# Optimization experiments

Hardware: AMD Instinct MI355X
Metric: run time of the kernel (lower is better)

## Reference

```python
import jax, jax.numpy as jnp
import numpy as np

B, NR, NA, NF = 2, 768, 768, 16
RIN, AIN = 1024, 1024
DIM, HEADS, DHEAD, DEPTH = 512, 8, 64, 4
INNER = HEADS * DHEAD
IFF = int(DIM * 4 * 2 / 3)  # 1365, GEGLU inner dim


def _ln(x, g, b=None):
    mu = jnp.mean(x, axis=-1, keepdims=True)
    var = jnp.mean((x - mu) ** 2, axis=-1, keepdims=True)
    y = (x - mu) * jax.lax.rsqrt(var + 1e-5) * g
    return y if b is None else y + b


def _heads(t):
    b, n, _ = t.shape
    return t.reshape(b, n, HEADS, DHEAD).transpose(0, 2, 1, 3)  # b h n d


def _attend(qx, kvx, wq, wkv, wo, mask):
    q = _heads(qx @ wq) * (DHEAD ** -0.5)
    k, v = map(_heads, jnp.split(kvx @ wkv, 2, axis=-1))
    sim = jnp.einsum('bhid,bhjd->bhij', q, k)
    sim = jnp.where(mask, sim, -jnp.finfo(sim.dtype).max)
    attn = jax.nn.softmax(sim, axis=-1)
    out = jnp.einsum('bhij,bhjd->bhid', attn, v)
    out = out.transpose(0, 2, 1, 3).reshape(qx.shape[0], -1, INNER)
    return out @ wo


def _masks():
    # token types: RNA=0, FUSION=2, ATAC=1, laid out [rna | fusion | atac]
    types = jnp.concatenate([jnp.zeros(NR, jnp.int32), jnp.full((NF,), 2, jnp.int32), jnp.ones(NA, jnp.int32)])
    same = (types[:, None] == types[None, :]).astype(jnp.int32)
    # replicates torch source precedence: (zorro_mask | types_from) == FUSION
    zorro = (same | types[:, None]) == 2
    rt = jnp.arange(3, dtype=jnp.int32)  # return token types (RNA, ATAC, FUSION)
    pm = (rt[:, None] == types[None, :]).astype(jnp.int32)
    # replicates source precedence: (pool_mask | return_types) == GLOBAL(3)
    pool = (pm | rt[:, None]) == 3
    return zorro[None, None], pool[None, None]


def setup_inputs() -> dict:
    key = jax.random.key(0)
    ks = jax.random.split(key, 16)
    w = lambda k, s: jax.random.normal(k, s, jnp.float32) * 0.02
    return {
        'rna': jax.random.normal(ks[0], (B, NR, RIN), jnp.float32),
        'atac': jax.random.normal(ks[1], (B, NA, AIN), jnp.float32),
        'rna_ln1_g': jnp.ones((RIN,)), 'rna_ln1_b': jnp.zeros((RIN,)),
        'rna_w': w(ks[2], (RIN, DIM)), 'rna_b': jnp.zeros((DIM,)),
        'rna_ln2_g': jnp.ones((DIM,)), 'rna_ln2_b': jnp.zeros((DIM,)),
        'atac_ln1_g': jnp.ones((AIN,)), 'atac_ln1_b': jnp.zeros((AIN,)),
        'atac_w': w(ks[3], (AIN, DIM)), 'atac_b': jnp.zeros((DIM,)),
        'atac_ln2_g': jnp.ones((DIM,)), 'atac_ln2_b': jnp.zeros((DIM,)),
        'fusion_tokens': jax.random.normal(ks[4], (NF, DIM), jnp.float32),
        'layers_attn_g': jnp.ones((DEPTH, DIM)),
        'layers_wq': w(ks[5], (DEPTH, DIM, INNER)),
        'layers_wkv': w(ks[6], (DEPTH, DIM, 2 * INNER)),
        'layers_wo': w(ks[7], (DEPTH, INNER, DIM)),
        'layers_ff_g': jnp.ones((DEPTH, DIM)),
        'layers_ff_w1': w(ks[8], (DEPTH, DIM, 2 * IFF)),
        'layers_ff_w2': w(ks[9], (DEPTH, IFF, DIM)),
        'final_g': jnp.ones((DIM,)),
        'return_tokens': jax.random.normal(ks[10], (3, DIM), jnp.float32),
        'pool_g': jnp.ones((DIM,)),
        'pool_wq': w(ks[11], (DIM, INNER)),
        'pool_wkv': w(ks[12], (DIM, 2 * INNER)),
        'pool_wo': w(ks[13], (INNER, DIM)),
    }


def reference(rna, atac, rna_ln1_g, rna_ln1_b, rna_w, rna_b, rna_ln2_g, rna_ln2_b,
              atac_ln1_g, atac_ln1_b, atac_w, atac_b, atac_ln2_g, atac_ln2_b,
              fusion_tokens, layers_attn_g, layers_wq, layers_wkv, layers_wo,
              layers_ff_g, layers_ff_w1, layers_ff_w2, final_g, return_tokens,
              pool_g, pool_wq, pool_wkv, pool_wo):
    zorro_mask, pool_mask = _masks()
    rna_tok = _ln(_ln(rna, rna_ln1_g, rna_ln1_b) @ rna_w + rna_b, rna_ln2_g, rna_ln2_b)
    atac_tok = _ln(_ln(atac, atac_ln1_g, atac_ln1_b) @ atac_w + atac_b, atac_ln2_g, atac_ln2_b)
    fus = jnp.broadcast_to(fusion_tokens, (B, NF, DIM))
    tokens = jnp.concatenate([rna_tok, fus, atac_tok], axis=1)  # [B, N, DIM]

    def layer(tok, p):
        ag, wq, wkv, wo, fg, w1, w2 = p
        xn = _ln(tok, ag)
        tok = tok + _attend(xn, xn, wq, wkv, wo, zorro_mask)
        h = _ln(tok, fg) @ w1
        x1, gate = jnp.split(h, 2, axis=-1)
        tok = tok + (jax.nn.gelu(gate, approximate=False) * x1) @ w2
        return tok, None

    tokens, _ = jax.lax.scan(layer, tokens,
                             (layers_attn_g, layers_wq, layers_wkv, layers_wo,
                              layers_ff_g, layers_ff_w1, layers_ff_w2))
    tokens = _ln(tokens, final_g)
    ret = jnp.broadcast_to(return_tokens, (B, 3, DIM))
    pooled = _attend(_ln(ret, pool_g), tokens, pool_wq, pool_wkv, pool_wo, pool_mask) + ret
    return pooled
```

## Files before the change

### kernel.cpp

```cpp
#include <hip/hip_runtime.h>
#include <stdint.h>
#include <stddef.h>

#define NTOK 1552
#define DIMM 512
#define IFFC 1365
#define IFF2 2730
#define NW1 2816
#define GSTRIDE 1408
#define BATCH 2
#define MALL (BATCH*NTOK)
#define AZ 6

typedef unsigned short u16;
typedef __attribute__((ext_vector_type(8))) short bf16x8;
typedef __attribute__((ext_vector_type(4))) float f32x4;

__device__ __forceinline__ u16 f2bf(float f){
  union { float f; uint32_t u; } v; v.f = f;
  uint32_t u = v.u;
  uint32_t r = (u + 0x7FFFu + ((u >> 16) & 1u)) >> 16;
  return (u16)r;
}
__device__ __forceinline__ float bf2f(u16 x){
  union { uint32_t u; float f; } v; v.u = ((uint32_t)x) << 16; return v.f;
}

__device__ __forceinline__ void gload_lds16(const u16* g, u16* l){
  __builtin_amdgcn_global_load_lds((const __attribute__((address_space(1))) void*)g,
                                   (__attribute__((address_space(3))) void*)l, 16, 0, 0);
}

__global__ void convall(const float* s0,const float* s1,const float* s2,const float* s3,
                        const float* s4,const float* s5,const float* s6,const float* s7,
                        u16* d0,u16* d1,u16* d2,u16* d3,u16* d4,u16* d5,u16* d6,u16* d7)
{
  const float* srcs[8] = {s0,s1,s2,s3,s4,s5,s6,s7};
  u16* dsts[8] = {d0,d1,d2,d3,d4,d5,d6,d7};
  const int KT[8]   = {32,32,16,16,16,16,44,16};
  const int NT[8]   = {16,16,32,16,16,88,16,32};
  const int TC[8]   = {512,512,2048,1024,1024,5632,2816,512};
  const int K_[8]   = {1024,1024,512,512,512,512,1365,512};
  const int NSRC[8] = {512,512,1024,512,512,2730,512,1024};
  const int LDK[8]  = {1024,1024,512,512,512,512,1408,512};
  const int NOUT[8] = {512,512,1024,512,512,2816,512,1024};
  const int WS_[8]  = {0,0,512*1024,512*512,512*512,512*2730,1365*512,0};
  const int WT_[8]  = {0,0,1024*512,512*512,512*512,2816*512,512*1408,0};

  int bid = blockIdx.x;
  int seg = 0, base = 0;
  while (seg < 7 && bid >= base + TC[seg]) { base += TC[seg]; ++seg; }
  int loc = bid - base;
  int kt = KT[seg];
  int z = loc / (kt*NT[seg]); loc -= z*(kt*NT[seg]);
  int kb = (loc % kt) * 32, nb = (loc / kt) * 32;
  const float* w = srcs[seg] + (size_t)z * WS_[seg];
  u16* wt = dsts[seg] + (size_t)z * WT_[seg];
  int K = K_[seg], NS = NSRC[seg], ldk = LDK[seg], NO = NOUT[seg];

  __shared__ float tile[32][33];
  int t = threadIdx.x;
  {
    int k = t >> 3, n4 = (t & 7) * 4;
    int gk = kb + k;
    float4 v = make_float4(0.f,0.f,0.f,0.f);
    if (gk < K){
      if (seg != 5){
        int gn = nb + n4;
        if (gn + 4 <= NS){
          v = *(const float4*)(w + (size_t)gk*NS + gn);
        } else {
          float* pv = (float*)&v;
          #pragma unroll
          for (int i = 0; i < 4; ++i){ int n = gn + i; if (n < NS) pv[i] = w[(size_t)gk*NS + n]; }
        }
      } else {
        float* pv = (float*)&v;
        #pragma unroll
        for (int i = 0; i < 4; ++i){
          int n = nb + n4 + i;
          if (n < NO){
            int bb = n >> 7, rr = n & 127, g = rr >> 5, hh = rr & 31;
            int j = bb*64 + g*16 + (hh & 15);
            if (j < 1365) pv[i] = w[(size_t)gk*NS + ((hh < 16) ? j : 1365 + j)];
          }
        }
      }
    }
    tile[k][n4] = v.x; tile[k][n4+1] = v.y; tile[k][n4+2] = v.z; tile[k][n4+3] = v.w;
  }
  __syncthreads();
  if (t < 128){
    int n = t >> 2, k8 = (t & 3) * 8;
    int gn = nb + n, gk = kb + k8;
    if (gn < NO && gk < ldk){
      u16 sh[8];
      #pragma unroll
      for (int i = 0; i < 8; ++i) sh[i] = f2bf(tile[k8+i][n]);
      *(bf16x8*)(wt + (size_t)gn*ldk + gk) = *(bf16x8*)sh;
    }
  }
}

__global__ void ln_kernel(const float* __restrict__ in, const float* __restrict__ g,
                          const float* __restrict__ bta, float* __restrict__ of32,
                          u16* __restrict__ obf, int D)
{
  const int r = blockIdx.x;
  const float* x = in + (size_t)r * D;
  float s = 0.f, ss = 0.f;
  for (int c = threadIdx.x; c < D; c += 256){ float v = x[c]; s += v; ss += v*v; }
  #pragma unroll
  for (int off = 32; off >= 1; off >>= 1){ s += __shfl_xor(s, off); ss += __shfl_xor(ss, off); }
  __shared__ float rs_[4], rss_[4];
  int w = threadIdx.x >> 6;
  if ((threadIdx.x & 63) == 0){ rs_[w] = s; rss_[w] = ss; }
  __syncthreads();
  s = rs_[0] + rs_[1] + rs_[2] + rs_[3];
  ss = rss_[0] + rss_[1] + rss_[2] + rss_[3];
  float mu = s / D;
  float rstd = rsqrtf(ss / D - mu*mu + 1e-5f);
  for (int c = threadIdx.x; c < D; c += 256){
    float y = (x[c] - mu) * rstd * g[c] + (bta ? bta[c] : 0.f);
    if (of32) of32[(size_t)r*D + c] = y;
    if (obf)  obf[(size_t)r*D + c] = f2bf(y);
  }
}

__global__ void embed_ln1(const float* __restrict__ rna, const float* __restrict__ atac,
                          const float* __restrict__ g0, const float* __restrict__ b0,
                          const float* __restrict__ g1, const float* __restrict__ b1,
                          u16* __restrict__ out)
{
  int r = blockIdx.x;
  const float* x; const float* g; const float* bb;
  if (r < 1536){ x = rna + (size_t)r*1024; g = g0; bb = b0; }
  else { x = atac + (size_t)(r-1536)*1024; g = g1; bb = b1; }
  float s = 0.f, ss = 0.f;
  int t = threadIdx.x;
  float v0 = x[t], v1 = x[t+256], v2 = x[t+512], v3 = x[t+768];
  s = v0+v1+v2+v3; ss = v0*v0+v1*v1+v2*v2+v3*v3;
  #pragma unroll
  for (int off = 32; off >= 1; off >>= 1){ s += __shfl_xor(s, off); ss += __shfl_xor(ss, off); }
  __shared__ float rs_[4], rss_[4];
  int w = t >> 6;
  if ((t & 63) == 0){ rs_[w] = s; rss_[w] = ss; }
  __syncthreads();
  s = rs_[0]+rs_[1]+rs_[2]+rs_[3];
  ss = rss_[0]+rss_[1]+rss_[2]+rss_[3];
  float mu = s / 1024.f;
  float rstd = rsqrtf(ss / 1024.f - mu*mu + 1e-5f);
  u16* o = out + (size_t)r*1024;
  o[t]     = f2bf((v0-mu)*rstd*g[t]     + bb[t]);
  o[t+256] = f2bf((v1-mu)*rstd*g[t+256] + bb[t+256]);
  o[t+512] = f2bf((v2-mu)*rstd*g[t+512] + bb[t+512]);
  o[t+768] = f2bf((v3-mu)*rstd*g[t+768] + bb[t+768]);
}

__global__ void embed_addln2(const float* __restrict__ part,
                             const float* __restrict__ rb, const float* __restrict__ ab,
                             const float* __restrict__ g0, const float* __restrict__ bt0,
                             const float* __restrict__ g1, const float* __restrict__ bt1,
                             float* __restrict__ tok)
{
  int r = blockIdx.x;
  int mod = (r >= 1536);
  int rl = mod ? r - 1536 : r;
  int b = rl / 768, rr = rl % 768;
  const float* bias = mod ? ab : rb;
  const float* g = mod ? g1 : g0;
  const float* bt = mod ? bt1 : bt0;
  const float* p0 = part + (size_t)r*DIMM;
  const float* p1 = p0 + (size_t)3072*DIMM;
  int t = threadIdx.x;
  float v0 = p0[t] + p1[t] + bias[t];
  float v1 = p0[t+256] + p1[t+256] + bias[t+256];
  float s = v0 + v1, ss = v0*v0 + v1*v1;
  #pragma unroll
  for (int off = 32; off >= 1; off >>= 1){ s += __shfl_xor(s, off); ss += __shfl_xor(ss, off); }
  __shared__ float rs_[4], rss_[4];
  int w = t >> 6;
  if ((t & 63) == 0){ rs_[w] = s; rss_[w] = ss; }
  __syncthreads();
  s = rs_[0]+rs_[1]+rs_[2]+rs_[3];
  ss = rss_[0]+rss_[1]+rss_[2]+rss_[3];
  float mu = s / DIMM;
  float rstd = rsqrtf(ss / DIMM - mu*mu + 1e-5f);
  float* tr = tok + ((size_t)(b*NTOK + (mod ? 784 : 0) + rr))*DIMM;
  tr[t]     = (v0 - mu)*rstd*g[t]     + bt[t];
  tr[t+256] = (v1 - mu)*rstd*g[t+256] + bt[t+256];
}

__global__ void resadd_ffnln(float* __restrict__ tok, const float* __restrict__ proj,
                             const float* __restrict__ g, u16* __restrict__ xn)
{
  int n = blockIdx.x, b = blockIdx.y;
  int pr = (n >= 768 && n < 784) ? (1 + n - 768) : 0;
  const float* p = proj + ((size_t)b*17 + pr)*DIMM;
  size_t row = (size_t)(b*NTOK + n)*DIMM;
  int t = threadIdx.x;
  float v0 = tok[row + t]     + p[t];
  float v1 = tok[row + t+256] + p[t+256];
  tok[row + t] = v0; tok[row + t+256] = v1;
  float s = v0 + v1, ss = v0*v0 + v1*v1;
  #pragma unroll
  for (int off = 32; off >= 1; off >>= 1){ s += __shfl_xor(s, off); ss += __shfl_xor(ss, off); }
  __shared__ float rs_[4], rss_[4];
  int w = t >> 6;
  if ((t & 63) == 0){ rs_[w] = s; rss_[w] = ss; }
  __syncthreads();
  s = rs_[0]+rs_[1]+rs_[2]+rs_[3];
  ss = rss_[0]+rss_[1]+rss_[2]+rss_[3];
  float mu = s / DIMM;
  float rstd = rsqrtf(ss / DIMM - mu*mu + 1e-5f);
  xn[row + t]     = f2bf((v0 - mu)*rstd*g[t]);
  xn[row + t+256] = f2bf((v1 - mu)*rstd*g[t+256]);
}

__global__ void skadd_ln(float* __restrict__ tok, const float* __restrict__ part,
                         const float* __restrict__ g, u16* __restrict__ xn)
{
  int r = blockIdx.x;
  size_t row = (size_t)r*DIMM;
  const float* p0 = part + row;
  const float* p1 = p0 + (size_t)MALL*DIMM;
  int t = threadIdx.x;
  float v0 = tok[row + t]     + p0[t]     + p1[t];
  float v1 = tok[row + t+256] + p0[t+256] + p1[t+256];
  tok[row + t] = v0; tok[row + t+256] = v1;
  float s = v0 + v1, ss = v0*v0 + v1*v1;
  #pragma unroll
  for (int off = 32; off >= 1; off >>= 1){ s += __shfl_xor(s, off); ss += __shfl_xor(ss, off); }
  __shared__ float rs_[4], rss_[4];
  int w = t >> 6;
  if ((t & 63) == 0){ rs_[w] = s; rss_[w] = ss; }
  __syncthreads();
  s = rs_[0]+rs_[1]+rs_[2]+rs_[3];
  ss = rss_[0]+rss_[1]+rss_[2]+rss_[3];
  float mu = s / DIMM;
  float rstd = rsqrtf(ss / DIMM - mu*mu + 1e-5f);
  xn[row + t]     = f2bf((v0 - mu)*rstd*g[t]);
  xn[row + t+256] = f2bf((v1 - mu)*rstd*g[t+256]);
}

__global__ __launch_bounds__(512) void gemm512(
    const u16* __restrict__ A, int lda,
    const u16* __restrict__ Bt, const u16* __restrict__ BtB, int mswitch, int ldk,
    float* __restrict__ C, int ldc, size_t Cz,
    u16* __restrict__ gout, float* __restrict__ csum,
    int M, int Nn, int K, int kchunk)
{
  __shared__ __align__(16) u16 As_lin[128*32];
  __shared__ __align__(16) u16 Bs_lin[128*32];
  __shared__ float colsum[2][128];
  const int t = threadIdx.x;
  const int lane = t & 63;
  const int w = t >> 6;
  const int wr = (w >> 2) * 64;
  const int wc = (w & 3) * 32;
  const int row0 = blockIdx.x * 128, col0 = blockIdx.y * 128;
  if (BtB && row0 >= mswitch) Bt = BtB;
  const int z = blockIdx.z;
  const int kbeg = z * kchunk;
  const int kend = (kbeg + kchunk < K) ? (kbeg + kchunk) : K;
  C += (size_t)z * Cz;
  const int l15 = lane & 15;
  const int l4 = (lane >> 4) * 8;
  const int sr = t >> 2, sc8 = (t & 3) * 8;
  int gr_s = row0 + sr; if (gr_s >= M) gr_s = M - 1;
  int gc_s = col0 + sr; if (gc_s >= Nn) gc_s = Nn - 1;
  const u16* Ag = A + (size_t)gr_s*lda + sc8;
  const u16* Bg = Bt + (size_t)gc_s*ldk + sc8;
  u16* Al = &As_lin[(size_t)w * 512];
  u16* Bl = &Bs_lin[(size_t)w * 512];

  f32x4 acc[4][2];
  #pragma unroll
  for (int m = 0; m < 4; ++m)
    #pragma unroll
    for (int n = 0; n < 2; ++n)
      #pragma unroll
      for (int j = 0; j < 4; ++j) acc[m][n][j] = 0.f;

  for (int k0 = kbeg; k0 < kend; k0 += 32) {
    gload_lds16(Ag + k0, Al);
    gload_lds16(Bg + k0, Bl);
    __syncthreads();
    bf16x8 af[4], bfr[2];
    #pragma unroll
    for (int m = 0; m < 4; ++m) af[m]  = *(const bf16x8*)(&As_lin[(wr + m*16 + l15)*32 + l4]);
    #pragma unroll
    for (int n = 0; n < 2; ++n) bfr[n] = *(const bf16x8*)(&Bs_lin[(wc + n*16 + l15)*32 + l4]);
    #pragma unroll
    for (int m = 0; m < 4; ++m)
      #pragma unroll
      for (int n = 0; n < 2; ++n)
        acc[m][n] = __builtin_amdgcn_mfma_f32_16x16x32_bf16(af[m], bfr[n], acc[m][n], 0, 0, 0);
    __syncthreads();
  }
  const int rb = (lane >> 4) * 4;
  if (gout){
    int jcol = (col0 >> 1) + (w & 3)*16 + l15;
    #pragma unroll
    for (int m = 0; m < 4; ++m){
      int gr0 = row0 + wr + m*16 + rb;
      #pragma unroll
      for (int j = 0; j < 4; ++j){
        int gr = gr0 + j;
        if (gr < M){
          float gt = acc[m][1][j];
          float ge = 0.5f * gt * (1.0f + erff(gt * 0.70710678118654752f));
          gout[(size_t)gr*GSTRIDE + jcol] = f2bf(ge * acc[m][0][j]);
        }
      }
    }
  } else {
    #pragma unroll
    for (int m = 0; m < 4; ++m){
      int gr0 = row0 + wr + m*16 + rb;
      #pragma unroll
      for (int n = 0; n < 2; ++n){
        int gc = col0 + wc + n*16 + l15;
        if (gc >= Nn) continue;
        #pragma unroll
        for (int j = 0; j < 4; ++j){
          int gr = gr0 + j;
          if (gr < M) C[(size_t)gr*ldc + gc] = acc[m][n][j];
        }
      }
    }
  }
  if (csum && col0 >= 512){
    if (t < 256) colsum[t>>7][t&127] = 0.f;
    __syncthreads();
    #pragma unroll
    for (int n = 0; n < 2; ++n){
      float lv0 = 0.f, lv1 = 0.f;
      #pragma unroll
      for (int m = 0; m < 4; ++m){
        int gr0 = row0 + wr + m*16 + rb;
        #pragma unroll
        for (int j = 0; j < 4; ++j){
          float v = acc[m][n][j];
          if (gr0 + j < NTOK) lv0 += v; else lv1 += v;
        }
      }
      int lc = wc + n*16 + l15;
      atomicAdd(&colsum[0][lc], lv0);
      atomicAdd(&colsum[1][lc], lv1);
    }
    __syncthreads();
    if (t < 256){
      int bb = t>>7, c = t&127;
      csum[((size_t)(bb*25) + blockIdx.x)*512 + (col0 - 512) + c] = colsum[bb][c];
    }
  }
}

__global__ __launch_bounds__(256) void gemm_tiny(
    const u16* __restrict__ A, int lda, size_t Abat,
    const u16* __restrict__ Bt, int ldk,
    float* __restrict__ C, int ldc, size_t Cbat,
    int M, int Nn, int K)
{
  A += (size_t)blockIdx.z * Abat;
  C += (size_t)blockIdx.z * Cbat;
  __shared__ __align__(16) u16 As[128][40];
  __shared__ __align__(16) u16 Bs[128][40];
  const int t = threadIdx.x;
  const int lane = t & 63;
  const int w = t >> 6;
  const int wr = (w >> 1) * 64, wc = (w & 1) * 64;
  const int col0 = blockIdx.y * 128;
  const int l15 = lane & 15;
  const int l4 = (lane >> 4) * 8;
  f32x4 acc[4][4];
  #pragma unroll
  for (int m = 0; m < 4; ++m)
    #pragma unroll
    for (int n = 0; n < 4; ++n)
      #pragma unroll
      for (int j = 0; j < 4; ++j) acc[m][n][j] = 0.f;

  for (int k0 = 0; k0 < K; k0 += 32) {
    #pragma unroll
    for (int u = 0; u < 2; ++u){
      int id = t + u*256;
      int r = id >> 2, c8 = (id & 3) * 8;
      bf16x8 av;
      #pragma unroll
      for (int j = 0; j < 8; ++j) av[j] = 0;
      if (r < M) av = *(const bf16x8*)(A + (size_t)r*lda + k0 + c8);
      *(bf16x8*)(&As[r][c8]) = av;
    }
    {
      int col = t & 127, kb = (t >> 7) * 16;
      bf16x8 b0, b1;
      #pragma unroll
      for (int j = 0; j < 8; ++j){ b0[j] = 0; b1[j] = 0; }
      int gc = col0 + col;
      if (gc < Nn){
        b0 = *(const bf16x8*)(Bt + (size_t)gc*ldk + k0 + kb);
        b1 = *(const bf16x8*)(Bt + (size_t)gc*ldk + k0 + kb + 8);
      }
      *(bf16x8*)(&Bs[col][kb])     = b0;
      *(bf16x8*)(&Bs[col][kb + 8]) = b1;
    }
    __syncthreads();
    bf16x8 af[4], bfr[4];
    #pragma unroll
    for (int m = 0; m < 4; ++m) af[m]  = *(const bf16x8*)(&As[wr + m*16 + l15][l4]);
    #pragma unroll
    for (int n = 0; n < 4; ++n) bfr[n] = *(const bf16x8*)(&Bs[wc + n*16 + l15][l4]);
    #pragma unroll
    for (int m = 0; m < 4; ++m)
      #pragma unroll
      for (int n = 0; n < 4; ++n)
        acc[m][n] = __builtin_amdgcn_mfma_f32_16x16x32_bf16(af[m], bfr[n], acc[m][n], 0, 0, 0);
    __syncthreads();
  }
  const int rb = (lane >> 4) * 4;
  #pragma unroll
  for (int m = 0; m < 4; ++m){
    int gr0 = wr + m*16 + rb;
    #pragma unroll
    for (int n = 0; n < 4; ++n){
      int gc = col0 + wc + n*16 + l15;
      if (gc >= Nn) continue;
      #pragma unroll
      for (int j = 0; j < 4; ++j){
        int gr = gr0 + j;
        if (gr < M) C[(size_t)gr*ldc + gc] = acc[m][n][j];
      }
    }
  }
}

__global__ __launch_bounds__(256) void fused_attn(
    const u16* __restrict__ xn, const u16* __restrict__ wqt,
    const float* __restrict__ kv, float* __restrict__ apart)
{
  int h = blockIdx.x, b = blockIdx.y;
  int qi = blockIdx.z / AZ, jz = blockIdx.z % AZ;
  int t = threadIdx.x;
  int lane = t & 63, wid = t >> 6;
  __shared__ float xs[512];
  __shared__ float qs[64];
  __shared__ float pl[256];
  __shared__ float red[4][64];
  __shared__ float redm[4];

  {
    int row = b*NTOK + 768 + qi;
    const u16* xr = xn + (size_t)row*DIMM;
    xs[t] = bf2f(xr[t]);
    xs[t+256] = bf2f(xr[t+256]);
  }
  __syncthreads();

  {
    const u16* wrr = wqt + (size_t)(h*64 + lane)*DIMM + wid*128;
    float a = 0.f;
    #pragma unroll
    for (int k = 0; k < 128; k += 8){
      bf16x8 wv = *(const bf16x8*)(wrr + k);
      int kb = wid*128 + k;
      #pragma unroll
      for (int i = 0; i < 8; ++i) a += xs[kb+i] * bf2f((u16)wv[i]);
    }
    red[wid][lane] = a;
  }
  __syncthreads();
  if (t < 64) qs[t] = (red[0][t] + red[1][t] + red[2][t] + red[3][t]) * 0.125f;
  __syncthreads();

  int jj = jz*256 + t;
  int j = (jj < 768) ? jj : jj + 16;
  float a = 0.f;
  {
    const float* kr = kv + ((size_t)(b*NTOK + j))*1024 + h*64;
    #pragma unroll
    for (int d = 0; d < 64; d += 4){
      float4 kd = *(const float4*)(kr + d);
      a += qs[d]*kd.x + qs[d+1]*kd.y + qs[d+2]*kd.z + qs[d+3]*kd.w;
    }
  }

  float m = a;
  #pragma unroll
  for (int off = 32; off >= 1; off >>= 1) m = fmaxf(m, __shfl_xor(m, off));
  if (lane == 0) redm[wid] = m;
  __syncthreads();
  m = fmaxf(fmaxf(redm[0], redm[1]), fmaxf(redm[2], redm[3]));
  float p = __expf(a - m);
  pl[t] = p;
  float sq = p;
  #pragma unroll
  for (int off = 32; off >= 1; off >>= 1) sq += __shfl_xor(sq, off);
  if (lane == 0) redm[wid] = sq;
  __syncthreads();

  {
    int j0 = wid * 64;
    const float* vb = kv + ((size_t)(b*NTOK + jz*256 + j0 + ((jz*256 + j0 >= 768) ? 16 : 0)))*1024
                      + 512 + h*64 + lane;
    float a0=0.f, a1=0.f, a2=0.f, a3=0.f;
    #pragma unroll 4
    for (int i = 0; i < 64; i += 4){
      const float* vp = vb + (size_t)i*1024;
      a0 += pl[j0+i]   * vp[0];
      a1 += pl[j0+i+1] * vp[1024];
      a2 += pl[j0+i+2] * vp[2048];
      a3 += pl[j0+i+3] * vp[3072];
    }
    red[wid][lane] = a0+a1+a2+a3;
  }
  __syncthreads();
  float* po = apart + ((((size_t)jz*BATCH + b)*8 + h)*16 + qi) * 68;
  if (t < 64) po[t] = red[0][t] + red[1][t] + red[2][t] + red[3][t];
  else if (t == 64) po[64] = m;
  else if (t == 65) po[65] = redm[0] + redm[1] + redm[2] + redm[3];
}

__global__ void attn_merge(const float* __restrict__ apart, const float* __restrict__ csum,
                           u16* __restrict__ zb)
{
  int bid = blockIdx.x, t = threadIdx.x;
  if (bid < 64){
    int i = bid*256 + t;
    int d = i & 63; int rest = i >> 6;
    int qi = rest & 15; int h = (rest >> 4) & 7; int b = rest >> 7;
    size_t base = ((size_t)b*8 + h)*16 + qi;
    float mz[AZ], sz[AZ];
    float M = -3.4e38f;
    #pragma unroll
    for (int z = 0; z < AZ; ++z){
      const float* po = apart + ((size_t)z*BATCH*8*16 + base) * 68;
      mz[z] = po[64]; sz[z] = po[65];
      M = fmaxf(M, mz[z]);
    }
    float S = 0.f, O = 0.f;
    #pragma unroll
    for (int z = 0; z < AZ; ++z){
      const float* po = apart + ((size_t)z*BATCH*8*16 + base) * 68;
      float w = __expf(mz[z] - M);
      S += sz[z] * w;
      O += po[d] * w;
    }
    zb[((size_t)(b*17 + 1 + qi))*DIMM + h*64 + d] = f2bf(O / S);
  } else {
    int i = (bid - 64)*256 + t;
    if (i >= BATCH*DIMM) return;
    int b = i >> 9, c = i & 511;
    float s = 0.f;
    #pragma unroll
    for (int bx = 0; bx < 25; ++bx) s += csum[((size_t)(b*25) + bx)*512 + c];
    zb[((size_t)(b*17))*DIMM + c] = f2bf(s * (1.0f/1552.0f));
  }
}

__global__ void csum_finish(const float* __restrict__ csum, float* __restrict__ mv)
{
  int i = blockIdx.x * 256 + threadIdx.x;
  if (i >= BATCH*DIMM) return;
  int b = i >> 9, c = i & 511;
  float s = 0.f;
  #pragma unroll
  for (int bx = 0; bx < 25; ++bx) s += csum[((size_t)(b*25) + bx)*512 + c];
  mv[(size_t)b*DIMM + c] = s * (1.0f/1552.0f);
}

__global__ void fuscopy_kernel(const float* __restrict__ ft, float* __restrict__ tok)
{
  int i = blockIdx.x * 256 + threadIdx.x;
  if (i >= BATCH*16*DIMM) return;
  int c = i & 511; int tt = i >> 9; int b = tt >> 4; int r = tt & 15;
  tok[((size_t)(b*NTOK + 768 + r))*DIMM + c] = ft[r*DIMM + c];
}

__global__ void matvec512(const float* __restrict__ y, const float* __restrict__ w,
                          float* __restrict__ out, float scale)
{
  __shared__ float ys[512];
  __shared__ float red[4][64];
  int t = threadIdx.x;
  ys[t] = y[t]; ys[t+256] = y[t+256];
  __syncthreads();
  int col = blockIdx.x*64 + (t & 63);
  int kq = t >> 6;
  float s = 0.f;
  #pragma unroll 4
  for (int k = kq*128; k < kq*128+128; ++k) s += ys[k] * w[(size_t)k*512 + col];
  red[kq][t & 63] = s;
  __syncthreads();
  if (t < 64)
    out[blockIdx.x*64 + t] = (red[0][t]+red[1][t]+red[2][t]+red[3][t]) * scale;
}

__global__ void pooledmv(const float* __restrict__ mv, const float* __restrict__ out2,
                         const float* __restrict__ wo, const float* __restrict__ rt,
                         float* __restrict__ out)
{
  int br = blockIdx.y; int b = br/3, r = br%3;
  const float* y = (r < 2) ? (mv + (size_t)b*DIMM) : (out2 + (size_t)b*DIMM);
  __shared__ float ys[512];
  __shared__ float red[4][64];
  int t = threadIdx.x;
  ys[t] = y[t]; ys[t+256] = y[t+256];
  __syncthreads();
  int col = blockIdx.x*64 + (t & 63);
  int kq = t >> 6;
  float s = 0.f;
  #pragma unroll 4
  for (int k = kq*128; k < kq*128+128; ++k) s += ys[k] * wo[(size_t)k*512 + col];
  red[kq][t & 63] = s;
  __syncthreads();
  if (t < 64){
    int c = blockIdx.x*64 + t;
    out[(size_t)br*DIMM + c] = red[0][t]+red[1][t]+red[2][t]+red[3][t] + rt[(size_t)r*DIMM + c];
  }
}

__global__ void poolattn2_kernel(const float* __restrict__ kv, const float* __restrict__ q2,
                                 float* __restrict__ out2)
{
  int h = blockIdx.x, b = blockIdx.y, d = threadIdx.x;
  __shared__ float sm[16];
  if (d < 16){
    const float* kr = kv + ((size_t)(b*NTOK + 768 + d))*1024 + h*64;
    float a = 0.f;
    for (int k = 0; k < 64; ++k) a += q2[h*64 + k] * kr[k];
    sm[d] = a;
  }
  __syncthreads();
  float m = -3.4e38f;
  #pragma unroll
  for (int j = 0; j < 16; ++j) m = fmaxf(m, sm[j]);
  float wv[16]; float s = 0.f;
  #pragma unroll
  for (int j = 0; j < 16; ++j){ wv[j] = expf(sm[j] - m); s += wv[j]; }
  float inv = 1.0f / s;
  float a = 0.f;
  #pragma unroll
  for (int j = 0; j < 16; ++j)
    a += wv[j] * kv[((size_t)(b*NTOK + 768 + j))*1024 + 512 + h*64 + d];
  out2[(size_t)b*DIMM + h*64 + d] = a * inv;
}

extern "C" void kernel_launch(void* const* d_in, const int* in_sizes, int n_in,
                              void* d_out, int out_size, void* d_ws, size_t ws_size,
                              hipStream_t stream)
{
  const float* rna        = (const float*)d_in[0];
  const float* atac       = (const float*)d_in[1];
  const float* rna_ln1_g  = (const float*)d_in[2];
  const float* rna_ln1_b  = (const float*)d_in[3];
  const float* rna_w      = (const float*)d_in[4];
  const float* rna_b      = (const float*)d_in[5];
  const float* rna_ln2_g  = (const float*)d_in[6];
  const float* rna_ln2_b  = (const float*)d_in[7];
  const float* atac_ln1_g = (const float*)d_in[8];
  const float* atac_ln1_b = (const float*)d_in[9];
  const float* atac_w     = (const float*)d_in[10];
  const float* atac_b     = (const float*)d_in[11];
  const float* atac_ln2_g = (const float*)d_in[12];
  const float* atac_ln2_b = (const float*)d_in[13];
  const float* fusion_tok = (const float*)d_in[14];
  const float* lay_ag     = (const float*)d_in[15];
  const float* lay_wq     = (const float*)d_in[16];
  const float* lay_wkv    = (const float*)d_in[17];
  const float* lay_wo     = (const float*)d_in[18];
  const float* lay_fg     = (const float*)d_in[19];
  const float* lay_w1     = (const float*)d_in[20];
  const float* lay_w2     = (const float*)d_in[21];
  const float* final_g    = (const float*)d_in[22];
  const float* ret_tok    = (const float*)d_in[23];
  const float* pool_g     = (const float*)d_in[24];
  const float* pool_wq    = (const float*)d_in[25];
  const float* pool_wkv   = (const float*)d_in[26];
  const float* pool_wo    = (const float*)d_in[27];

  uint8_t* ws = (uint8_t*)d_ws;
  size_t off = 0;
  auto carve = [&](size_t bytes) -> uint8_t* {
    uint8_t* p = ws + off;
    off += (bytes + 255) & ~(size_t)255;
    return p;
  };
  u16* rna_wt   = (u16*)carve((size_t)512*1024*2);
  u16* atac_wt  = (u16*)carve((size_t)512*1024*2);
  u16* wkvt     = (u16*)carve((size_t)4*1024*512*2);
  u16* wqt      = (u16*)carve((size_t)4*512*512*2);
  u16* wot      = (u16*)carve((size_t)4*512*512*2);
  u16* w1t      = (u16*)carve((size_t)4*NW1*512*2);
  u16* w2t      = (u16*)carve((size_t)4*512*GSTRIDE*2);
  u16* pool_wkvt= (u16*)carve((size_t)1024*512*2);
  float* tok   = (float*)carve((size_t)MALL * DIMM * 4);
  u16*   xn    = (u16*)  carve((size_t)MALL * DIMM * 2);
  float* kv    = (float*)carve((size_t)MALL * 1024 * 4);
  u16*   lnbuf = (u16*)  carve((size_t)3072 * 1024 * 2);
  u16*   zb    = (u16*)  carve((size_t)BATCH*17*DIMM * 2);
  float* proj  = (float*)carve((size_t)BATCH*17*DIMM * 4);
  float* mv    = (float*)carve((size_t)BATCH*DIMM * 4);
  float* q2    = (float*)carve((size_t)DIMM * 4);
  float* yq2   = (float*)carve((size_t)DIMM * 4);
  float* out2  = (float*)carve((size_t)BATCH*DIMM * 4);
  float* csum  = (float*)carve((size_t)BATCH*25*512 * 4);
  float* apart = (float*)carve((size_t)AZ*BATCH*8*16*68 * 4);
  u16*   gbuf  = (u16*)  carve((size_t)MALL * GSTRIDE * 2);
  float* skpart= (float*)carve((size_t)2 * MALL * 512 * 4);
  (void)ws_size;

  convall<<<14080, 256, 0, stream>>>(rna_w, atac_w, lay_wkv, lay_wq, lay_wo, lay_w1, lay_w2, pool_wkv,
                                     rna_wt, atac_wt, wkvt, wqt, wot, w1t, w2t, pool_wkvt);

  embed_ln1<<<3072, 256, 0, stream>>>(rna, atac, rna_ln1_g, rna_ln1_b, atac_ln1_g, atac_ln1_b, lnbuf);
  gemm512<<<dim3(24, 4, 2), 512, 0, stream>>>(lnbuf, 1024, rna_wt, atac_wt, 1536, 1024,
                                              skpart, 512, (size_t)3072*512, nullptr, nullptr,
                                              3072, 512, 1024, 512);
  embed_addln2<<<3072, 256, 0, stream>>>(skpart, rna_b, atac_b, rna_ln2_g, rna_ln2_b,
                                         atac_ln2_g, atac_ln2_b, tok);
  fuscopy_kernel<<<(BATCH*16*DIMM + 255)/256, 256, 0, stream>>>(fusion_tok, tok);

  ln_kernel<<<MALL, 256, 0, stream>>>(tok, lay_ag, nullptr, nullptr, xn, 512);

  for (int l = 0; l < 4; ++l){
    const float* fg  = lay_fg + (size_t)l*DIMM;
    const float* gnext = (l < 3) ? (lay_ag + (size_t)(l+1)*DIMM) : final_g;
    const u16* wkvt_l = wkvt + (size_t)l*1024*512;
    const u16* wqt_l  = wqt  + (size_t)l*512*512;
    const u16* wot_l  = wot  + (size_t)l*512*512;
    const u16* w1t_l  = w1t  + (size_t)l*NW1*512;
    const u16* w2t_l  = w2t  + (size_t)l*512*GSTRIDE;

    gemm512<<<dim3(25, 8, 1), 512, 0, stream>>>(xn, 512, wkvt_l, nullptr, 0, 512,
                                                kv, 1024, 0, nullptr, csum, MALL, 1024, 512, 512);
    fused_attn<<<dim3(8, BATCH, 16*AZ), 256, 0, stream>>>(xn, wqt_l, kv, apart);
    attn_merge<<<68, 256, 0, stream>>>(apart, csum, zb);
    gemm_tiny<<<dim3(1, 4, 2), 256, 0, stream>>>(zb, 512, (size_t)17*DIMM,
                                                 wot_l, 512, proj, 512, (size_t)17*DIMM, 17, 512, 512);
    resadd_ffnln<<<dim3(NTOK, BATCH), 256, 0, stream>>>(tok, proj, fg, xn);
    gemm512<<<dim3(25, 22, 1), 512, 0, stream>>>(xn, 512, w1t_l, nullptr, 0, 512,
                                                 nullptr, 0, 0, gbuf, nullptr, MALL, NW1, 512, 512);
    gemm512<<<dim3(25, 4, 2), 512, 0, stream>>>(gbuf, GSTRIDE, w2t_l, nullptr, 0, GSTRIDE,
                                                skpart, 512, (size_t)MALL*512, nullptr, nullptr,
                                                MALL, 512, GSTRIDE, 704);
    skadd_ln<<<MALL, 256, 0, stream>>>(tok, skpart, gnext, xn);
  }

  gemm512<<<dim3(25, 8, 1), 512, 0, stream>>>(xn, 512, pool_wkvt, nullptr, 0, 512,
                                              kv, 1024, 0, nullptr, csum, MALL, 1024, 512, 512);
  csum_finish<<<4, 256, 0, stream>>>(csum, mv);
  ln_kernel<<<1, 256, 0, stream>>>(ret_tok + 2*DIMM, pool_g, nullptr, yq2, nullptr, 512);
  matvec512<<<8, 256, 0, stream>>>(yq2, pool_wq, q2, 0.125f);
  poolattn2_kernel<<<dim3(8, BATCH), 64, 0, stream>>>(kv, q2, out2);
  pooledmv<<<dim3(8, 6), 256, 0, stream>>>(mv, out2, pool_wo, ret_tok, (float*)d_out);
}
```

Before: 563.3 us.

## Fuse small kernels: embed LN chain, attention merge with out-proj, pooling tail

The first layer's attention LayerNorm now runs inside embed_addln2 and a new fuscopy_ln kernel, so the separate ln_kernel pass over all tokens is gone. attn_merge and gemm_tiny become one attn_out kernel that merges the partial softmax results into shared memory and does the 17-row output projection as a matvec. The five pooling-tail kernels collapse into one pool_final kernel. Together this removes about three launches per layer plus several at the start and end, and some global round-trips. The trade-off is that pool_final recomputes the q projection redundantly in every block, and the output projection now reads fp32 values where the old path rounded them to bf16 first.

```diff
diff --git a/kernel.cpp b/kernel.cpp
--- a/kernel.cpp
+++ b/kernel.cpp
@@ -102,31 +102,6 @@
   }
 }
 
-__global__ void ln_kernel(const float* __restrict__ in, const float* __restrict__ g,
-                          const float* __restrict__ bta, float* __restrict__ of32,
-                          u16* __restrict__ obf, int D)
-{
-  const int r = blockIdx.x;
-  const float* x = in + (size_t)r * D;
-  float s = 0.f, ss = 0.f;
-  for (int c = threadIdx.x; c < D; c += 256){ float v = x[c]; s += v; ss += v*v; }
-  #pragma unroll
-  for (int off = 32; off >= 1; off >>= 1){ s += __shfl_xor(s, off); ss += __shfl_xor(ss, off); }
-  __shared__ float rs_[4], rss_[4];
-  int w = threadIdx.x >> 6;
-  if ((threadIdx.x & 63) == 0){ rs_[w] = s; rss_[w] = ss; }
-  __syncthreads();
-  s = rs_[0] + rs_[1] + rs_[2] + rs_[3];
-  ss = rss_[0] + rss_[1] + rss_[2] + rss_[3];
-  float mu = s / D;
-  float rstd = rsqrtf(ss / D - mu*mu + 1e-5f);
-  for (int c = threadIdx.x; c < D; c += 256){
-    float y = (x[c] - mu) * rstd * g[c] + (bta ? bta[c] : 0.f);
-    if (of32) of32[(size_t)r*D + c] = y;
-    if (obf)  obf[(size_t)r*D + c] = f2bf(y);
-  }
-}
-
 __global__ void embed_ln1(const float* __restrict__ rna, const float* __restrict__ atac,
                           const float* __restrict__ g0, const float* __restrict__ b0,
                           const float* __restrict__ g1, const float* __restrict__ b1,
@@ -161,7 +136,8 @@
                              const float* __restrict__ rb, const float* __restrict__ ab,
                              const float* __restrict__ g0, const float* __restrict__ bt0,
                              const float* __restrict__ g1, const float* __restrict__ bt1,
-                             float* __restrict__ tok)
+                             const float* __restrict__ ag0,
+                             float* __restrict__ tok, u16* __restrict__ xn)
 {
   int r = blockIdx.x;
   int mod = (r >= 1536);
@@ -186,9 +162,47 @@
   ss = rss_[0]+rss_[1]+rss_[2]+rss_[3];
   float mu = s / DIMM;
   float rstd = rsqrtf(ss / DIMM - mu*mu + 1e-5f);
-  float* tr = tok + ((size_t)(b*NTOK + (mod ? 784 : 0) + rr))*DIMM;
-  tr[t]     = (v0 - mu)*rstd*g[t]     + bt[t];
-  tr[t+256] = (v1 - mu)*rstd*g[t+256] + bt[t+256];
+  size_t row = (size_t)(b*NTOK + (mod ? 784 : 0) + rr)*DIMM;
+  float t0 = (v0 - mu)*rstd*g[t]     + bt[t];
+  float t1 = (v1 - mu)*rstd*g[t+256] + bt[t+256];
+  tok[row + t] = t0; tok[row + t+256] = t1;
+  float s2 = t0 + t1, ss2 = t0*t0 + t1*t1;
+  #pragma unroll
+  for (int off = 32; off >= 1; off >>= 1){ s2 += __shfl_xor(s2, off); ss2 += __shfl_xor(ss2, off); }
+  __syncthreads();
+  if ((t & 63) == 0){ rs_[w] = s2; rss_[w] = ss2; }
+  __syncthreads();
+  s2 = rs_[0]+rs_[1]+rs_[2]+rs_[3];
+  ss2 = rss_[0]+rss_[1]+rss_[2]+rss_[3];
+  float mu2 = s2 / DIMM;
+  float rstd2 = rsqrtf(ss2 / DIMM - mu2*mu2 + 1e-5f);
+  xn[row + t]     = f2bf((t0 - mu2)*rstd2*ag0[t]);
+  xn[row + t+256] = f2bf((t1 - mu2)*rstd2*ag0[t+256]);
+}
+
+__global__ void fuscopy_ln(const float* __restrict__ ft, const float* __restrict__ ag0,
+                           float* __restrict__ tok, u16* __restrict__ xn)
+{
+  int bid = blockIdx.x;
+  int b = bid >> 4, rr = bid & 15;
+  int t = threadIdx.x;
+  const float* x = ft + (size_t)rr*DIMM;
+  float v0 = x[t], v1 = x[t+256];
+  size_t row = (size_t)(b*NTOK + 768 + rr)*DIMM;
+  tok[row + t] = v0; tok[row + t+256] = v1;
+  float s = v0 + v1, ss = v0*v0 + v1*v1;
+  #pragma unroll
+  for (int off = 32; off >= 1; off >>= 1){ s += __shfl_xor(s, off); ss += __shfl_xor(ss, off); }
+  __shared__ float rs_[4], rss_[4];
+  int w = t >> 6;
+  if ((t & 63) == 0){ rs_[w] = s; rss_[w] = ss; }
+  __syncthreads();
+  s = rs_[0]+rs_[1]+rs_[2]+rs_[3];
+  ss = rss_[0]+rss_[1]+rss_[2]+rss_[3];
+  float mu = s / DIMM;
+  float rstd = rsqrtf(ss / DIMM - mu*mu + 1e-5f);
+  xn[row + t]     = f2bf((v0 - mu)*rstd*ag0[t]);
+  xn[row + t+256] = f2bf((v1 - mu)*rstd*ag0[t+256]);
 }
 
 __global__ void resadd_ffnln(float* __restrict__ tok, const float* __restrict__ proj,
@@ -357,85 +371,6 @@
   }
 }
 
-__global__ __launch_bounds__(256) void gemm_tiny(
-    const u16* __restrict__ A, int lda, size_t Abat,
-    const u16* __restrict__ Bt, int ldk,
-    float* __restrict__ C, int ldc, size_t Cbat,
-    int M, int Nn, int K)
-{
-  A += (size_t)blockIdx.z * Abat;
-  C += (size_t)blockIdx.z * Cbat;
-  __shared__ __align__(16) u16 As[128][40];
-  __shared__ __align__(16) u16 Bs[128][40];
-  const int t = threadIdx.x;
-  const int lane = t & 63;
-  const int w = t >> 6;
-  const int wr = (w >> 1) * 64, wc = (w & 1) * 64;
-  const int col0 = blockIdx.y * 128;
-  const int l15 = lane & 15;
-  const int l4 = (lane >> 4) * 8;
-  f32x4 acc[4][4];
-  #pragma unroll
-  for (int m = 0; m < 4; ++m)
-    #pragma unroll
-    for (int n = 0; n < 4; ++n)
-      #pragma unroll
-      for (int j = 0; j < 4; ++j) acc[m][n][j] = 0.f;
-
-  for (int k0 = 0; k0 < K; k0 += 32) {
-    #pragma unroll
-    for (int u = 0; u < 2; ++u){
-      int id = t + u*256;
-      int r = id >> 2, c8 = (id & 3) * 8;
-      bf16x8 av;
-      #pragma unroll
-      for (int j = 0; j < 8; ++j) av[j] = 0;
-      if (r < M) av = *(const bf16x8*)(A + (size_t)r*lda + k0 + c8);
-      *(bf16x8*)(&As[r][c8]) = av;
-    }
-    {
-      int col = t & 127, kb = (t >> 7) * 16;
-      bf16x8 b0, b1;
-      #pragma unroll
-      for (int j = 0; j < 8; ++j){ b0[j] = 0; b1[j] = 0; }
-      int gc = col0 + col;
-      if (gc < Nn){
-        b0 = *(const bf16x8*)(Bt + (size_t)gc*ldk + k0 + kb);
-        b1 = *(const bf16x8*)(Bt + (size_t)gc*ldk + k0 + kb + 8);
-      }
-      *(bf16x8*)(&Bs[col][kb])     = b0;
-      *(bf16x8*)(&Bs[col][kb + 8]) = b1;
-    }
-    __syncthreads();
-    bf16x8 af[4], bfr[4];
-    #pragma unroll
-    for (int m = 0; m < 4; ++m) af[m]  = *(const bf16x8*)(&As[wr + m*16 + l15][l4]);
-    #pragma unroll
-    for (int n = 0; n < 4; ++n) bfr[n] = *(const bf16x8*)(&Bs[wc + n*16 + l15][l4]);
-    #pragma unroll
-    for (int m = 0; m < 4; ++m)
-      #pragma unroll
-      for (int n = 0; n < 4; ++n)
-        acc[m][n] = __builtin_amdgcn_mfma_f32_16x16x32_bf16(af[m], bfr[n], acc[m][n], 0, 0, 0);
-    __syncthreads();
-  }
-  const int rb = (lane >> 4) * 4;
-  #pragma unroll
-  for (int m = 0; m < 4; ++m){
-    int gr0 = wr + m*16 + rb;
-    #pragma unroll
-    for (int n = 0; n < 4; ++n){
-      int gc = col0 + wc + n*16 + l15;
-      if (gc >= Nn) continue;
-      #pragma unroll
-      for (int j = 0; j < 4; ++j){
-        int gr = gr0 + j;
-        if (gr < M) C[(size_t)gr*ldc + gc] = acc[m][n][j];
-      }
-    }
-  }
-}
-
 __global__ __launch_bounds__(256) void fused_attn(
     const u16* __restrict__ xn, const u16* __restrict__ wqt,
     const float* __restrict__ kv, float* __restrict__ apart)
@@ -522,129 +457,174 @@
   else if (t == 65) po[65] = redm[0] + redm[1] + redm[2] + redm[3];
 }
 
-__global__ void attn_merge(const float* __restrict__ apart, const float* __restrict__ csum,
-                           u16* __restrict__ zb)
-{
-  int bid = blockIdx.x, t = threadIdx.x;
-  if (bid < 64){
-    int i = bid*256 + t;
-    int d = i & 63; int rest = i >> 6;
-    int qi = rest & 15; int h = (rest >> 4) & 7; int b = rest >> 7;
-    size_t base = ((size_t)b*8 + h)*16 + qi;
-    float mz[AZ], sz[AZ];
-    float M = -3.4e38f;
-    #pragma unroll
-    for (int z = 0; z < AZ; ++z){
-      const float* po = apart + ((size_t)z*BATCH*8*16 + base) * 68;
-      mz[z] = po[64]; sz[z] = po[65];
-      M = fmaxf(M, mz[z]);
-    }
-    float S = 0.f, O = 0.f;
-    #pragma unroll
-    for (int z = 0; z < AZ; ++z){
-      const float* po = apart + ((size_t)z*BATCH*8*16 + base) * 68;
-      float w = __expf(mz[z] - M);
-      S += sz[z] * w;
-      O += po[d] * w;
-    }
-    zb[((size_t)(b*17 + 1 + qi))*DIMM + h*64 + d] = f2bf(O / S);
+__global__ __launch_bounds__(256) void attn_out(
+    const float* __restrict__ apart, const float* __restrict__ csum,
+    const u16* __restrict__ wot, float* __restrict__ proj)
+{
+  int colchunk = blockIdx.x;
+  int b = blockIdx.y;
+  int rg = blockIdx.z;
+  int r0 = (rg == 0) ? 0 : (1 + 4*rg);
+  int nr = (rg == 0) ? 5 : 4;
+  __shared__ float zbl[5][512];
+  __shared__ float red[4][64];
+  int t = threadIdx.x;
+
+  for (int rr = 0; rr < nr; ++rr){
+    int r = r0 + rr;
+    if (r == 0){
+      for (int c = t; c < 512; c += 256){
+        float s = 0.f;
+        #pragma unroll
+        for (int bx = 0; bx < 25; ++bx) s += csum[((size_t)(b*25)+bx)*512 + c];
+        zbl[rr][c] = s * (1.0f/1552.0f);
+      }
+    } else {
+      int qi = r - 1;
+      for (int c = t; c < 512; c += 256){
+        int h = c >> 6, d = c & 63;
+        size_t base = ((size_t)b*8 + h)*16 + qi;
+        float mz[AZ], sz[AZ];
+        float M = -3.4e38f;
+        #pragma unroll
+        for (int z = 0; z < AZ; ++z){
+          const float* po = apart + ((size_t)z*BATCH*8*16 + base)*68;
+          mz[z] = po[64]; sz[z] = po[65];
+          M = fmaxf(M, mz[z]);
+        }
+        float S = 0.f, O = 0.f;
+        #pragma unroll
+        for (int z = 0; z < AZ; ++z){
+          const float* po = apart + ((size_t)z*BATCH*8*16 + base)*68;
+          float wz = __expf(mz[z] - M);
+          S += sz[z]*wz; O += po[d]*wz;
+        }
+        zbl[rr][c] = O / S;
+      }
+    }
+  }
+  __syncthreads();
+
+  int col = colchunk*64 + (t & 63);
+  int kq = t >> 6;
+  const u16* wrow = wot + (size_t)col*512 + kq*128;
+  for (int rr = 0; rr < nr; ++rr){
+    float a = 0.f;
+    #pragma unroll
+    for (int k = 0; k < 128; k += 8){
+      bf16x8 wv = *(const bf16x8*)(wrow + k);
+      #pragma unroll
+      for (int i = 0; i < 8; ++i) a += zbl[rr][kq*128 + k + i] * bf2f((u16)wv[i]);
+    }
+    red[kq][t & 63] = a;
+    __syncthreads();
+    if (t < 64)
+      proj[((size_t)(b*17) + r0 + rr)*DIMM + colchunk*64 + t] =
+        red[0][t] + red[1][t] + red[2][t] + red[3][t];
+    __syncthreads();
+  }
+}
+
+__global__ __launch_bounds__(256) void pool_final(
+    const float* __restrict__ csum, const float* __restrict__ rt,
+    const float* __restrict__ pg, const float* __restrict__ wq,
+    const float* __restrict__ kv, const float* __restrict__ wo,
+    float* __restrict__ out)
+{
+  int colchunk = blockIdx.x;
+  int br = blockIdx.y; int b = br/3, r = br%3;
+  __shared__ float ys[512];
+  __shared__ float q2l[512];
+  __shared__ float sm[8][16];
+  __shared__ float pn[8][16];
+  __shared__ float red[4][64];
+  __shared__ float rs_[4], rss_[4];
+  int t = threadIdx.x;
+
+  if (r < 2){
+    float a0 = 0.f, a1 = 0.f;
+    #pragma unroll
+    for (int bx = 0; bx < 25; ++bx){
+      a0 += csum[((size_t)(b*25)+bx)*512 + t];
+      a1 += csum[((size_t)(b*25)+bx)*512 + t + 256];
+    }
+    ys[t] = a0 * (1.0f/1552.0f);
+    ys[t+256] = a1 * (1.0f/1552.0f);
+    __syncthreads();
   } else {
-    int i = (bid - 64)*256 + t;
-    if (i >= BATCH*DIMM) return;
-    int b = i >> 9, c = i & 511;
-    float s = 0.f;
-    #pragma unroll
-    for (int bx = 0; bx < 25; ++bx) s += csum[((size_t)(b*25) + bx)*512 + c];
-    zb[((size_t)(b*17))*DIMM + c] = f2bf(s * (1.0f/1552.0f));
-  }
-}
-
-__global__ void csum_finish(const float* __restrict__ csum, float* __restrict__ mv)
-{
-  int i = blockIdx.x * 256 + threadIdx.x;
-  if (i >= BATCH*DIMM) return;
-  int b = i >> 9, c = i & 511;
-  float s = 0.f;
-  #pragma unroll
-  for (int bx = 0; bx < 25; ++bx) s += csum[((size_t)(b*25) + bx)*512 + c];
-  mv[(size_t)b*DIMM + c] = s * (1.0f/1552.0f);
-}
-
-__global__ void fuscopy_kernel(const float* __restrict__ ft, float* __restrict__ tok)
-{
-  int i = blockIdx.x * 256 + threadIdx.x;
-  if (i >= BATCH*16*DIMM) return;
-  int c = i & 511; int tt = i >> 9; int b = tt >> 4; int r = tt & 15;
-  tok[((size_t)(b*NTOK + 768 + r))*DIMM + c] = ft[r*DIMM + c];
-}
-
-__global__ void matvec512(const float* __restrict__ y, const float* __restrict__ w,
-                          float* __restrict__ out, float scale)
-{
-  __shared__ float ys[512];
-  __shared__ float red[4][64];
-  int t = threadIdx.x;
-  ys[t] = y[t]; ys[t+256] = y[t+256];
-  __syncthreads();
-  int col = blockIdx.x*64 + (t & 63);
+    const float* x = rt + 2*DIMM;
+    float v0 = x[t], v1 = x[t+256];
+    float s = v0 + v1, ss = v0*v0 + v1*v1;
+    #pragma unroll
+    for (int off = 32; off >= 1; off >>= 1){ s += __shfl_xor(s, off); ss += __shfl_xor(ss, off); }
+    int w = t >> 6;
+    if ((t & 63) == 0){ rs_[w] = s; rss_[w] = ss; }
+    __syncthreads();
+    s = rs_[0]+rs_[1]+rs_[2]+rs_[3];
+    ss = rss_[0]+rss_[1]+rss_[2]+rss_[3];
+    float mu = s / DIMM;
+    float rstd = rsqrtf(ss / DIMM - mu*mu + 1e-5f);
+    ys[t]     = (v0 - mu)*rstd*pg[t];
+    ys[t+256] = (v1 - mu)*rstd*pg[t+256];
+    __syncthreads();
+    {
+      float a0 = 0.f, a1 = 0.f;
+      for (int k = 0; k < 512; ++k){
+        float yv = ys[k];
+        a0 += yv * wq[(size_t)k*512 + t];
+        a1 += yv * wq[(size_t)k*512 + t + 256];
+      }
+      q2l[t] = a0 * 0.125f;
+      q2l[t+256] = a1 * 0.125f;
+    }
+    __syncthreads();
+    if (t < 128){
+      int h = t >> 4, j = t & 15;
+      const float* kr = kv + ((size_t)(b*NTOK + 768 + j))*1024 + h*64;
+      float a = 0.f;
+      #pragma unroll
+      for (int d = 0; d < 64; ++d) a += q2l[h*64 + d] * kr[d];
+      sm[h][j] = a;
+    }
+    __syncthreads();
+    if (t < 8){
+      float m = -3.4e38f;
+      #pragma unroll
+      for (int j = 0; j < 16; ++j) m = fmaxf(m, sm[t][j]);
+      float e[16]; float s2 = 0.f;
+      #pragma unroll
+      for (int j = 0; j < 16; ++j){ e[j] = __expf(sm[t][j] - m); s2 += e[j]; }
+      float inv = 1.0f / s2;
+      #pragma unroll
+      for (int j = 0; j < 16; ++j) pn[t][j] = e[j] * inv;
+    }
+    __syncthreads();
+    {
+      int c0 = t, c1 = t + 256;
+      int h0 = c0 >> 6, h1 = c1 >> 6;
+      float a0 = 0.f, a1 = 0.f;
+      #pragma unroll
+      for (int j = 0; j < 16; ++j){
+        const float* vr = kv + ((size_t)(b*NTOK + 768 + j))*1024 + 512;
+        a0 += pn[h0][j] * vr[c0];
+        a1 += pn[h1][j] * vr[c1];
+      }
+      ys[c0] = a0; ys[c1] = a1;
+    }
+    __syncthreads();
+  }
+
+  int col = colchunk*64 + (t & 63);
   int kq = t >> 6;
-  float s = 0.f;
+  float a = 0.f;
   #pragma unroll 4
-  for (int k = kq*128; k < kq*128+128; ++k) s += ys[k] * w[(size_t)k*512 + col];
-  red[kq][t & 63] = s;
-  __syncthreads();
-  if (t < 64)
-    out[blockIdx.x*64 + t] = (red[0][t]+red[1][t]+red[2][t]+red[3][t]) * scale;
-}
-
-__global__ void pooledmv(const float* __restrict__ mv, const float* __restrict__ out2,
-                         const float* __restrict__ wo, const float* __restrict__ rt,
-                         float* __restrict__ out)
-{
-  int br = blockIdx.y; int b = br/3, r = br%3;
-  const float* y = (r < 2) ? (mv + (size_t)b*DIMM) : (out2 + (size_t)b*DIMM);
-  __shared__ float ys[512];
-  __shared__ float red[4][64];
-  int t = threadIdx.x;
-  ys[t] = y[t]; ys[t+256] = y[t+256];
-  __syncthreads();
-  int col = blockIdx.x*64 + (t & 63);
-  int kq = t >> 6;
-  float s = 0.f;
-  #pragma unroll 4
-  for (int k = kq*128; k < kq*128+128; ++k) s += ys[k] * wo[(size_t)k*512 + col];
-  red[kq][t & 63] = s;
+  for (int k = kq*128; k < kq*128 + 128; ++k) a += ys[k] * wo[(size_t)k*512 + col];
+  red[kq][t & 63] = a;
   __syncthreads();
   if (t < 64){
-    int c = blockIdx.x*64 + t;
+    int c = colchunk*64 + t;
     out[(size_t)br*DIMM + c] = red[0][t]+red[1][t]+red[2][t]+red[3][t] + rt[(size_t)r*DIMM + c];
   }
-}
-
-__global__ void poolattn2_kernel(const float* __restrict__ kv, const float* __restrict__ q2,
-                                 float* __restrict__ out2)
-{
-  int h = blockIdx.x, b = blockIdx.y, d = threadIdx.x;
-  __shared__ float sm[16];
-  if (d < 16){
-    const float* kr = kv + ((size_t)(b*NTOK + 768 + d))*1024 + h*64;
-    float a = 0.f;
-    for (int k = 0; k < 64; ++k) a += q2[h*64 + k] * kr[k];
-    sm[d] = a;
-  }
-  __syncthreads();
-  float m = -3.4e38f;
-  #pragma unroll
-  for (int j = 0; j < 16; ++j) m = fmaxf(m, sm[j]);
-  float wv[16]; float s = 0.f;
-  #pragma unroll
-  for (int j = 0; j < 16; ++j){ wv[j] = expf(sm[j] - m); s += wv[j]; }
-  float inv = 1.0f / s;
-  float a = 0.f;
-  #pragma unroll
-  for (int j = 0; j < 16; ++j)
-    a += wv[j] * kv[((size_t)(b*NTOK + 768 + j))*1024 + 512 + h*64 + d];
-  out2[(size_t)b*DIMM + h*64 + d] = a * inv;
 }
 
 extern "C" void kernel_launch(void* const* d_in, const int* in_sizes, int n_in,
@@ -699,12 +679,7 @@
   u16*   xn    = (u16*)  carve((size_t)MALL * DIMM * 2);
   float* kv    = (float*)carve((size_t)MALL * 1024 * 4);
   u16*   lnbuf = (u16*)  carve((size_t)3072 * 1024 * 2);
-  u16*   zb    = (u16*)  carve((size_t)BATCH*17*DIMM * 2);
   float* proj  = (float*)carve((size_t)BATCH*17*DIMM * 4);
-  float* mv    = (float*)carve((size_t)BATCH*DIMM * 4);
-  float* q2    = (float*)carve((size_t)DIMM * 4);
-  float* yq2   = (float*)carve((size_t)DIMM * 4);
-  float* out2  = (float*)carve((size_t)BATCH*DIMM * 4);
   float* csum  = (float*)carve((size_t)BATCH*25*512 * 4);
   float* apart = (float*)carve((size_t)AZ*BATCH*8*16*68 * 4);
   u16*   gbuf  = (u16*)  carve((size_t)MALL * GSTRIDE * 2);
@@ -719,10 +694,8 @@
                                               skpart, 512, (size_t)3072*512, nullptr, nullptr,
                                               3072, 512, 1024, 512);
   embed_addln2<<<3072, 256, 0, stream>>>(skpart, rna_b, atac_b, rna_ln2_g, rna_ln2_b,
-                                         atac_ln2_g, atac_ln2_b, tok);
-  fuscopy_kernel<<<(BATCH*16*DIMM + 255)/256, 256, 0, stream>>>(fusion_tok, tok);
-
-  ln_kernel<<<MALL, 256, 0, stream>>>(tok, lay_ag, nullptr, nullptr, xn, 512);
+                                         atac_ln2_g, atac_ln2_b, lay_ag, tok, xn);
+  fuscopy_ln<<<32, 256, 0, stream>>>(fusion_tok, lay_ag, tok, xn);
 
   for (int l = 0; l < 4; ++l){
     const float* fg  = lay_fg + (size_t)l*DIMM;
@@ -736,9 +709,7 @@
     gemm512<<<dim3(25, 8, 1), 512, 0, stream>>>(xn, 512, wkvt_l, nullptr, 0, 512,
                                                 kv, 1024, 0, nullptr, csum, MALL, 1024, 512, 512);
     fused_attn<<<dim3(8, BATCH, 16*AZ), 256, 0, stream>>>(xn, wqt_l, kv, apart);
-    attn_merge<<<68, 256, 0, stream>>>(apart, csum, zb);
-    gemm_tiny<<<dim3(1, 4, 2), 256, 0, stream>>>(zb, 512, (size_t)17*DIMM,
-                                                 wot_l, 512, proj, 512, (size_t)17*DIMM, 17, 512, 512);
+    attn_out<<<dim3(8, BATCH, 4), 256, 0, stream>>>(apart, csum, wot_l, proj);
     resadd_ffnln<<<dim3(NTOK, BATCH), 256, 0, stream>>>(tok, proj, fg, xn);
     gemm512<<<dim3(25, 22, 1), 512, 0, stream>>>(xn, 512, w1t_l, nullptr, 0, 512,
                                                  nullptr, 0, 0, gbuf, nullptr, MALL, NW1, 512, 512);
@@ -750,9 +721,6 @@
 
   gemm512<<<dim3(25, 8, 1), 512, 0, stream>>>(xn, 512, pool_wkvt, nullptr, 0, 512,
                                               kv, 1024, 0, nullptr, csum, MALL, 1024, 512, 512);
-  csum_finish<<<4, 256, 0, stream>>>(csum, mv);
-  ln_kernel<<<1, 256, 0, stream>>>(ret_tok + 2*DIMM, pool_g, nullptr, yq2, nullptr, 512);
-  matvec512<<<8, 256, 0, stream>>>(yq2, pool_wq, q2, 0.125f);
-  poolattn2_kernel<<<dim3(8, BATCH), 64, 0, stream>>>(kv, q2, out2);
-  pooledmv<<<dim3(8, 6), 256, 0, stream>>>(mv, out2, pool_wo, ret_tok, (float*)d_out);
-}
+  pool_final<<<dim3(8, 6), 256, 0, stream>>>(csum, ret_tok, pool_g, pool_wq, kv, pool_wo,
+                                             (float*)d_out);
+}
```

Measured after the change: 561.9 us. Within noise of the previous version (-0.2%).
